# Optimization experiments

Measured on AMD Instinct MI355X. Metric: run time of the kernel, lower is better.

## Reference

```python
import jax, jax.numpy as jnp
import numpy as np

H_IMG = W_IMG = 1024
H_MAP = W_MAP = 64
SCALE = 16  # img // fmap, both axes
SCALES = [2, 2.5, 3, 3.5, 4, 5]
RATIOS = [0.5, 1.5, 2.0, 2.5, 3, 3.5, 4]
A = len(SCALES) * len(RATIOS)  # 42
POS_T, NEG_T = 0.5, 0.3


def _anchors_np():
    # generate_base_anchors + generate_anchor_boxes (down_h = down_w = SCALE)
    base = np.zeros((A, 4), np.float32)
    cy = cx = SCALE / 2.0
    i = 0
    for s in SCALES:
        for ar in RATIOS:
            h = SCALE * s * np.sqrt(ar)
            w = SCALE * s * np.sqrt(1.0 / ar)
            base[i] = [cy - h / 2.0, cx - w / 2.0, cy + h / 2.0, cx + w / 2.0]
            i += 1
    sy = np.arange(H_MAP) * SCALE
    sx = np.arange(W_MAP) * SCALE
    gx, gy = np.meshgrid(sx, sy)
    shifts = np.stack([gy.ravel(), gx.ravel(), gy.ravel(), gx.ravel()], axis=1)
    # order (H, W, A) -> matches conf.permute(0,2,3,1) flatten
    return (base[None, :, :] + shifts[:, None, :]).reshape(-1, 4).astype(np.float32)


def _conv(x, w, b):
    y = jax.lax.conv_general_dilated(x, w, (1, 1), 'SAME',
                                     dimension_numbers=('NCHW', 'OIHW', 'NCHW'))
    return y + b[None, :, None, None]


def setup_inputs() -> dict:
    key = jax.random.key(0)
    ks = jax.random.split(key, 10)
    B, N, C, Hm, Wm, HID = 8, 20, 256, 64, 64, 512
    feature_map = jax.random.normal(ks[0], (B, C, Hm, Wm), dtype=jnp.float32)
    # valid GT boxes in pixel xyxy-style (d0<d2, d1<d3), last 5 per image padded -1
    p0 = jax.random.uniform(ks[1], (B, N)) * 860.0
    p1 = jax.random.uniform(ks[2], (B, N)) * 860.0
    s0 = jax.random.uniform(ks[3], (B, N)) * 144.0 + 16.0
    s1 = jax.random.uniform(ks[4], (B, N)) * 144.0 + 16.0
    gt_bboxes = jnp.stack([p0, p1, p0 + s0, p1 + s1], axis=-1)
    gt_bboxes = gt_bboxes.at[:, 15:, :].set(-1.0)
    gt_classes = jax.random.randint(ks[5], (B, N), 0, 10)
    conv1_w = jax.random.normal(ks[6], (HID, C, 3, 3), dtype=jnp.float32) * 0.02
    conv1_b = jnp.zeros((HID,), jnp.float32)
    conf_w = jax.random.normal(ks[7], (A, HID, 1, 1), dtype=jnp.float32) * 0.02
    conf_b = jnp.zeros((A,), jnp.float32)
    reg_w = jax.random.normal(ks[8], (4 * A, HID, 1, 1), dtype=jnp.float32) * 0.02
    reg_b = jnp.zeros((4 * A,), jnp.float32)
    return {"feature_map": feature_map, "gt_bboxes": gt_bboxes, "gt_classes": gt_classes,
            "conv1_w": conv1_w, "conv1_b": conv1_b, "conf_w": conf_w, "conf_b": conf_b,
            "reg_w": reg_w, "reg_b": reg_b}


def reference(feature_map, gt_bboxes, gt_classes, conv1_w, conv1_b,
              conf_w, conf_b, reg_w, reg_b):
    anc = jnp.asarray(_anchors_np())           # [M,4]
    B = feature_map.shape[0]
    M = anc.shape[0]                           # H*W*A

    # project_bboxes p2a: divide by scale, keep -1 padding
    pad = gt_bboxes == -1.0
    g = jnp.where(pad, -1.0, gt_bboxes / float(SCALE))  # [B,N,4]
    valid = g[..., 0] >= 0                                # [B,N]
    g_safe = jnp.where(valid[..., None], g, jnp.array([0.0, 0.0, 1.0, 1.0]))

    # pairwise IoU [B,M,N] (vectorized get_iou_mat; invalid GT -> 0)
    tl = jnp.maximum(anc[None, :, None, :2], g_safe[:, None, :, :2])
    br = jnp.minimum(anc[None, :, None, 2:], g_safe[:, None, :, 2:])
    wh = jnp.clip(br - tl, 0.0)
    inter = wh[..., 0] * wh[..., 1]
    area_a = (anc[:, 2] - anc[:, 0]) * (anc[:, 3] - anc[:, 1])
    area_g = (g_safe[..., 2] - g_safe[..., 0]) * (g_safe[..., 3] - g_safe[..., 1])
    iou = inter / (area_a[None, :, None] + area_g[:, None, :] - inter)
    iou = jnp.where(valid[:, None, :], iou, 0.0)

    # positive assignment: per-GT argmax anchors + IoU > pos_thresh
    max_per_gt = iou.max(axis=1, keepdims=True)            # [B,1,N]
    pos_mask = ((iou == max_per_gt) & (max_per_gt > 0)) | (iou > POS_T)
    pos_any = pos_mask.any(axis=-1)                        # [B,M]
    a2g = jnp.argmax(iou, axis=2)                          # [B,M]
    max_per_anc = iou.max(axis=2)                          # [B,M]

    gt_for_anc = jnp.take_along_axis(g_safe, a2g[:, :, None], axis=1)  # [B,M,4]
    anc_b = jnp.broadcast_to(anc, (B, M, 4))
    gt_sel = jnp.where(pos_any[..., None], gt_for_anc, anc_b)  # safe for log

    # calc_gt_offsets (cxcywh encode), computed for all anchors, masked later
    a_c = (anc_b[..., :2] + anc_b[..., 2:]) * 0.5
    a_s = anc_b[..., 2:] - anc_b[..., :2]
    g_c = (gt_sel[..., :2] + gt_sel[..., 2:]) * 0.5
    g_s = gt_sel[..., 2:] - gt_sel[..., :2]
    off_gt = jnp.concatenate([(g_c - a_c) / a_s, jnp.log(g_s / a_s)], axis=-1)
    off_gt = off_gt.reshape(-1, 4)                          # [B*M,4]

    # ProposalModule head (dropout is a no-op in eval)
    x = jax.nn.relu(_conv(feature_map, conv1_w, conv1_b))
    conf = _conv(x, conf_w, conf_b)                         # [B,A,H,W]
    reg = _conv(x, reg_w, reg_b)                            # [B,4A,H,W]
    cflat = conf.transpose(0, 2, 3, 1).reshape(-1)          # [B*M]
    offp = reg.transpose(0, 2, 3, 1).reshape(-1, 4)         # [B*M,4]

    pf = pos_any.reshape(-1).astype(jnp.float32)
    P = pf.sum()

    # cls loss: BCE-with-logits, label 1 on positives, 0 on P sampled negatives
    cls_pos = (jax.nn.softplus(-cflat) * pf).sum() / P
    neg = max_per_anc.reshape(-1) < NEG_T
    scores = jax.random.uniform(jax.random.key(7), cflat.shape)
    scores = jnp.where(neg, scores, 2.0)
    ranks = jnp.argsort(jnp.argsort(scores))               # random sample = rank < P
    sel = (neg & (ranks < P)).astype(jnp.float32)
    cls_neg = (jax.nn.softplus(cflat) * sel).sum() / sel.sum()
    cls_loss = 0.5 * (cls_pos + cls_neg)

    d = offp - off_gt
    ad = jnp.abs(d)
    sl1 = jnp.where(ad < 1.0, 0.5 * ad * ad, ad - 0.5)
    reg_loss = (sl1 * pf[:, None]).sum() / (P * 4.0)

    return cls_loss + reg_loss
```

## Files before the change

### kernel.cpp

```cpp
#include <hip/hip_runtime.h>
#include <hip/hip_fp16.h>
#include <stdint.h>

constexpr int B_  = 8, HM = 64, WM = 64, A_ = 42, CIN = 256, HIDN = 512;
constexpr int M_  = HM * WM * A_;
constexpr int NA  = B_ * M_;
constexpr int HALF = NA / 2;
constexpr int KK  = CIN * 9;
constexpr float POS_T = 0.5f;

constexpr int WINY = 10, WINX = 10, WPIX = WINY * WINX;
constexpr int PERIMG = A_ * WPIX;
constexpr int WBLK = (PERIMG + 511) / 512;
constexpr int NMAXB = WBLK * B_;

constexpr int MAXPOS = 4096, MAXSEL = 4096, MAXCAND = 16384, MAXTIE = 256;
constexpr int MAXPIX = 1024;
constexpr uint32_t VCAND = 16384u;

constexpr int KSPL = 8, KCH = KK / KSPL;
constexpr int NSTRIP = MAXPIX / 64;
constexpr int NOCH = 4;
constexpr int NTILE = NSTRIP * NOCH * KSPL;
constexpr int TFBLK = HALF / 512;
constexpr int WCVTB = (HIDN * KK / 4) / 512;

constexpr size_t OFF_CTRL  = 0;
constexpr size_t OFF_BINS  = 256;
constexpr size_t OFF_MAXGT = 768;
constexpr size_t MS_END    = 1408;
constexpr size_t OFF_SLOT  = 2048;
constexpr size_t OFF_PLIST = 133120;
constexpr size_t OFF_POSL  = 137216;
constexpr size_t OFF_SELL  = 153600;
constexpr size_t OFF_CAND  = 169984;
constexpr size_t OFF_PART  = 301056;
constexpr size_t OFF_APATCH= 8689664;
constexpr size_t OFF_WF16  = 13408256;


__device__ __forceinline__ unsigned short f2bf(float f) {
  uint32_t x = __float_as_uint(f);
  uint32_t r = x + 0x7FFFu + ((x >> 16) & 1u);
  return (unsigned short)(r >> 16);
}
__device__ __forceinline__ float bf2f(unsigned short h) {
  return __uint_as_float(((uint32_t)h) << 16);
}
__device__ __forceinline__ uint32_t f2h2(float a, float b) {
  return (uint32_t)__half_as_ushort(__float2half_rn(a)) |
         ((uint32_t)__half_as_ushort(__float2half_rn(b)) << 16);
}

typedef _Float16 h8v __attribute__((ext_vector_type(8)));
typedef float f4v __attribute__((ext_vector_type(4)));

__device__ __forceinline__ float iou_pair(float ay0, float ax0, float ay1, float ax1,
                                          float areaA, float g0, float g1, float g2, float g3,
                                          float areaG) {
#pragma clang fp contract(off)
  float ty = fmaxf(ay0, g0), tx = fmaxf(ax0, g1);
  float by = fminf(ay1, g2), bx = fminf(ax1, g3);
  float hy = by - ty; hy = fmaxf(hy, 0.f);
  float hx = bx - tx; hx = fmaxf(hx, 0.f);
  float inter = hy * hx;
  return inter / (areaA + areaG - inter);
}

__device__ __forceinline__ void anchor_box(const float* basef, int a, int y, int x,
                                           float& ay0, float& ax0, float& ay1, float& ax1,
                                           float& areaA) {
#pragma clang fp contract(off)
  double sy = 16.0 * (double)y, sx = 16.0 * (double)x;
  ay0 = (float)((double)basef[a * 4 + 0] + sy);
  ax0 = (float)((double)basef[a * 4 + 1] + sx);
  ay1 = (float)((double)basef[a * 4 + 2] + sy);
  ax1 = (float)((double)basef[a * 4 + 3] + sx);
  areaA = (ay1 - ay0) * (ax1 - ax0);
}

__device__ __forceinline__ void fill_base(float* sbase, int t) {
  if (t < 42) {
    const double SC[6] = {2.0, 2.5, 3.0, 3.5, 4.0, 5.0};
    const double RA[7] = {0.5, 1.5, 2.0, 2.5, 3.0, 3.5, 4.0};
    int si = t / 7, ri = t - si * 7;
    double h = 16.0 * SC[si] * sqrt(RA[ri]);
    double w = 16.0 * SC[si] * sqrt(1.0 / RA[ri]);
    sbase[t * 4 + 0] = (float)(8.0 - h / 2.0);
    sbase[t * 4 + 1] = (float)(8.0 - w / 2.0);
    sbase[t * 4 + 2] = (float)(8.0 + h / 2.0);
    sbase[t * 4 + 3] = (float)(8.0 + w / 2.0);
  }
}

__device__ __forceinline__ void fill_gt(const float* gt, int b, float* sg, float* sarea,
                                        unsigned* sval, int t) {
  if (t < 20) {
#pragma clang fp contract(off)
    float g4[4];
    for (int d = 0; d < 4; d++) {
      float v = gt[(b * 20 + t) * 4 + d];
      g4[d] = (v == -1.0f) ? -1.0f : v * 0.0625f;
    }
    unsigned valid = (g4[0] >= 0.0f) ? 1u : 0u;
    if (!valid) { g4[0] = 0.f; g4[1] = 0.f; g4[2] = 1.f; g4[3] = 1.f; }
    sg[t * 4 + 0] = g4[0]; sg[t * 4 + 1] = g4[1]; sg[t * 4 + 2] = g4[2]; sg[t * 4 + 3] = g4[3];
    sarea[t] = (g4[2] - g4[0]) * (g4[3] - g4[1]);
    sval[t] = valid;
  }
}

__device__ __forceinline__ void claim_pixel(char* ws, int pixg) {
  int* slotmap = (int*)(ws + OFF_SLOT);
  if (atomicCAS((unsigned*)&slotmap[pixg], 0u, 0xFFFFFFFFu) == 0u) {
    unsigned s = atomicAdd((unsigned*)(ws + OFF_CTRL) + 2, 1u);
    if (s < MAXPIX) { ((int*)(ws + OFF_PLIST))[s] = pixg; slotmap[pixg] = (int)s + 1; }
    else slotmap[pixg] = -1;
  }
}

__device__ __forceinline__ float softplusf(float x) {
  return fmaxf(x, 0.f) + log1pf(expf(-fabsf(x)));
}
__device__ __forceinline__ float sl1(float d) {
  float ad = fabsf(d);
  return ad < 1.f ? 0.5f * ad * ad : ad - 0.5f;
}

__device__ __forceinline__ void tf_round(uint32_t& x0, uint32_t& x1, int r) {
  x0 += x1; x1 = (x1 << r) | (x1 >> (32 - r)); x1 ^= x0;
}
__device__ __forceinline__ void threefry(uint32_t c0, uint32_t c1, uint32_t& o0, uint32_t& o1) {
  const uint32_t k0 = 0u, k1 = 7u;
  const uint32_t k2 = k0 ^ k1 ^ 0x1BD11BDAu;
  uint32_t x0 = c0 + k0, x1 = c1 + k1;
  tf_round(x0, x1, 13); tf_round(x0, x1, 15); tf_round(x0, x1, 26); tf_round(x0, x1, 6);
  x0 += k1; x1 += k2 + 1u;
  tf_round(x0, x1, 17); tf_round(x0, x1, 29); tf_round(x0, x1, 16); tf_round(x0, x1, 24);
  x0 += k2; x1 += k0 + 2u;
  tf_round(x0, x1, 13); tf_round(x0, x1, 15); tf_round(x0, x1, 26); tf_round(x0, x1, 6);
  x0 += k0; x1 += k1 + 3u;
  tf_round(x0, x1, 17); tf_round(x0, x1, 29); tf_round(x0, x1, 16); tf_round(x0, x1, 24);
  x0 += k1; x1 += k2 + 4u;
  tf_round(x0, x1, 13); tf_round(x0, x1, 15); tf_round(x0, x1, 26); tf_round(x0, x1, 6);
  x0 += k2; x1 += k0 + 5u;
  o0 = x0; o1 = x1;
}

__device__ __forceinline__ void dev_threefry_emit(char* ws, int p) {
  uint32_t o0, o1; threefry((uint32_t)p, (uint32_t)(p + HALF), o0, o1);
  uint32_t v0 = o0 >> 9, v1 = o1 >> 9;
  unsigned* ctrl = (unsigned*)(ws + OFF_CTRL);
  unsigned* bins = (unsigned*)(ws + OFF_BINS);
  uint2* cand = (uint2*)(ws + OFF_CAND);
  if (v0 < VCAND) {
    unsigned s = atomicAdd(&ctrl[3], 1u);
    if (s < MAXCAND) cand[s] = make_uint2(v0, (unsigned)p);
    atomicAdd(&bins[v0 >> 7], 1u);
  }
  if (v1 < VCAND) {
    unsigned s = atomicAdd(&ctrl[3], 1u);
    if (s < MAXCAND) cand[s] = make_uint2(v1, (unsigned)(p + HALF));
    atomicAdd(&bins[v1 >> 7], 1u);
  }
}

__global__ void __launch_bounds__(512) kTF(const float* __restrict__ gt,
                                           const float* __restrict__ w1, char* ws) {
  __shared__ float sbase[168], sg[80], sarea[20];
  __shared__ unsigned sval[20];
  __shared__ int smax[20];
  int t = threadIdx.x;
  if (blockIdx.x < NMAXB) {
    int b = blockIdx.x / WBLK, blk = blockIdx.x - b * WBLK;
    fill_base(sbase, t);
    fill_gt(gt, b, sg, sarea, sval, t);
    if (t < 20) smax[t] = 0;
    __syncthreads();
    int idx = blk * 512 + t;
    bool ok = idx < PERIMG;
    float ay0 = 0.f, ax0 = 0.f, ay1 = 0.f, ax1 = 0.f, areaA = 1.f;
    if (ok) {
      int a = idx / WPIX, pp = idx - a * WPIX;
      int y = pp / WINX, x = pp - y * WINX;
      anchor_box(sbase, a, y, x, ay0, ax0, ay1, ax1, areaA);
    }
#pragma unroll
    for (int n = 0; n < 20; n++) {
      float io = 0.f;
      if (ok && sval[n]) io = iou_pair(ay0, ax0, ay1, ax1, areaA,
                                       sg[n * 4], sg[n * 4 + 1], sg[n * 4 + 2],
                                       sg[n * 4 + 3], sarea[n]);
#pragma unroll
      for (int off = 32; off >= 1; off >>= 1) io = fmaxf(io, __shfl_xor(io, off, 64));
      if ((t & 63) == 0 && io > 0.f) atomicMax(&smax[n], __float_as_int(io));
    }
    __syncthreads();
    if (t < 20 && smax[t] != 0)
      atomicMax((int*)(ws + OFF_MAXGT) + b * 20 + t, smax[t]);
  } else if (blockIdx.x < NMAXB + TFBLK) {
    int p = ((int)blockIdx.x - NMAXB) * 512 + t;
    if (p < 32768) ((int*)(ws + OFF_SLOT))[p] = 0;
    if (p < HALF) dev_threefry_emit(ws, p);
  } else {
    int q = ((int)blockIdx.x - (NMAXB + TFBLK)) * 512 + t;
    float4 v = ((const float4*)w1)[q];
    uint2 o;
    o.x = f2h2(v.x, v.y);
    o.y = f2h2(v.z, v.w);
    ((uint2*)(ws + OFF_WF16))[q] = o;
  }
}

__global__ void __launch_bounds__(512) kPos2(const float* __restrict__ gt, char* ws) {
  __shared__ float sbase[168], sg[80], sarea[20], smg[20];
  __shared__ unsigned sval[20];
  int b = blockIdx.y, t = threadIdx.x;
  unsigned* ctrl = (unsigned*)(ws + OFF_CTRL);
  fill_base(sbase, t);
  fill_gt(gt, b, sg, sarea, sval, t);
  if (t < 20) smg[t] = __int_as_float(((int*)(ws + OFF_MAXGT))[b * 20 + t]);
  __syncthreads();
  int idx = blockIdx.x * 512 + t;
  bool pos = false;
  unsigned packv = 0;
  int pixg = 0;
  if (idx < PERIMG) {
    int a = idx / WPIX, pp = idx - a * WPIX;
    int y = pp / WINX, x = pp - y * WINX;
    float ay0, ax0, ay1, ax1, areaA;
    anchor_box(sbase, a, y, x, ay0, ax0, ay1, ax1, areaA);
    float best = -1.f; int arg = 0;
#pragma unroll
    for (int n = 0; n < 20; n++) {
      float io = 0.f;
      if (sval[n]) io = iou_pair(ay0, ax0, ay1, ax1, areaA,
                                 sg[n * 4], sg[n * 4 + 1], sg[n * 4 + 2],
                                 sg[n * 4 + 3], sarea[n]);
      if (io > best) { best = io; arg = n; }
      float mg = smg[n];
      pos = pos || ((io == mg) && (mg > 0.f)) || (io > POS_T);
    }
    if (pos) {
      int pix = y * 64 + x;
      int i = b * M_ + pix * 42 + a;
      packv = (unsigned)i | ((unsigned)arg << 21);
      pixg = b * 4096 + pix;
    }
  }
  unsigned long long mask = __ballot(pos);
  if (mask) {
    int lane = t & 63;
    int leader = (int)__ffsll(mask) - 1;
    int cnt = __popcll(mask);
    unsigned base = 0;
    if (lane == leader) base = atomicAdd(&ctrl[0], (unsigned)cnt);
    base = (unsigned)__shfl((int)base, leader, 64);
    if (pos) {
      unsigned slot = base + (unsigned)__popcll(mask & ((1ull << lane) - 1ull));
      if (slot < MAXPOS) ((unsigned*)(ws + OFF_POSL))[slot] = packv;
      claim_pixel(ws, pixg);
    }
  }
}

__global__ void __launch_bounds__(1024) kSel(char* ws) {
  __shared__ unsigned selbins[128];
  __shared__ uint2 ties[MAXTIE];
  __shared__ unsigned tcnt, s_r, s_ucut;
  __shared__ int s_icut, s_cutbin;
  int t = threadIdx.x;
  unsigned* ctrl = (unsigned*)(ws + OFF_CTRL);
  const uint2* cand = (const uint2*)(ws + OFF_CAND);
  unsigned P = min(ctrl[0], (unsigned)MAXPOS);
  unsigned nc = min(ctrl[3], (unsigned)MAXCAND);
  if (t < 128) selbins[t] = ((const unsigned*)(ws + OFF_BINS))[t];
  if (t == 0) tcnt = 0;
  __syncthreads();
  if (t == 0) {
    unsigned cum = 0; int c = 0;
    for (; c < 128; c++) { if (cum + selbins[c] >= P) break; cum += selbins[c]; }
    if (c == 128) c = 127;
    s_cutbin = c; s_r = (P > cum) ? (P - cum) : 0u;
  }
  __syncthreads();
  int cutbin = s_cutbin;
  for (unsigned j = t; j < nc; j += 1024) {
    uint2 cj = cand[j];
    if ((int)(cj.x >> 7) == cutbin) {
      unsigned k = atomicAdd(&tcnt, 1u);
      if (k < MAXTIE) ties[k] = cj;
    }
  }
  __syncthreads();
  unsigned n = min(tcnt, (unsigned)MAXTIE);
  unsigned r = s_r; if (r > n) r = n;
  if (r == 0) {
    if (t == 0) { s_ucut = 0; s_icut = -1; }
  } else if (t < (int)n) {
    uint2 mine = ties[t];
    unsigned rank = 0;
    for (unsigned j = 0; j < n; j++) {
      uint2 o = ties[j];
      if (o.x < mine.x || (o.x == mine.x && (int)o.y < (int)mine.y)) rank++;
    }
    if (rank == r - 1) { s_ucut = mine.x; s_icut = (int)mine.y; }
  }
  __syncthreads();
  unsigned ucut = s_ucut; int icut = s_icut;
  unsigned total = (nc + 1023u) & ~1023u;
  for (unsigned j = t; j < total; j += 1024) {
    bool sel = false; uint2 cj = make_uint2(0u, 0u);
    if (j < nc) {
      cj = cand[j];
      sel = (cj.x < ucut) || (cj.x == ucut && (int)cj.y <= icut);
    }
    unsigned long long mask = __ballot(sel);
    if (mask) {
      int lane = t & 63;
      int leader = (int)__ffsll(mask) - 1;
      int cnt = __popcll(mask);
      unsigned base = 0;
      if (lane == leader) base = atomicAdd(&ctrl[1], (unsigned)cnt);
      base = (unsigned)__shfl((int)base, leader, 64);
      if (sel) {
        unsigned slot = base + (unsigned)__popcll(mask & ((1ull << lane) - 1ull));
        if (slot < MAXSEL) {
          ((int*)(ws + OFF_SELL))[slot] = (int)cj.y;
          int bb = (int)cj.y / M_; int m = (int)cj.y - bb * M_;
          claim_pixel(ws, bb * 4096 + m / 42);
        }
      }
    }
  }
}

__global__ void __launch_bounds__(256) kIm2col(const float* __restrict__ fm, char* ws) {
  unsigned* ctrl = (unsigned*)(ws + OFF_CTRL);
  int npix = min((int)ctrl[2], MAXPIX);
  int blk = blockIdx.x;
  if (blk >= npix) return;
  int chunk = blockIdx.y;
  int pixg = ((const int*)(ws + OFF_PLIST))[blk];
  int b = pixg >> 12, pix = pixg & 4095;
  int y = pix >> 6, x = pix & 63;
  uint32_t* Ap = (uint32_t*)(ws + OFF_APATCH) + (size_t)blk * (KK / 2);
  int u0 = chunk * 384;
  for (int u = u0 + threadIdx.x; u < u0 + 384; u += 256) {
    float v[2];
#pragma unroll
    for (int h = 0; h < 2; h++) {
      int k = 2 * u + h;
      int ic = k / 9, r = k - ic * 9;
      int dy = r / 3, dx = r - dy * 3;
      int yy = y + dy - 1, xx = x + dx - 1;
      float vv = 0.f;
      if (yy >= 0 && yy < 64 && xx >= 0 && xx < 64)
        vv = fm[(((size_t)b * CIN + ic) * 64 + yy) * 64 + xx];
      v[h] = vv;
    }
    Ap[u] = f2h2(v[0], v[1]);
  }
}

__global__ void __launch_bounds__(256) kGemm(char* ws) {
  unsigned* ctrl = (unsigned*)(ws + OFF_CTRL);
  int npix = min((int)ctrl[2], MAXPIX);
  int tile = blockIdx.x;
  int strip = tile & 15, r2 = tile >> 4;
  int och = r2 & 3, ks = r2 >> 2;
  int px0 = strip * 64;
  if (px0 >= npix) return;
  int oc0 = och * 128, kb = ks * KCH;
  const _Float16* Ap = (const _Float16*)(ws + OFF_APATCH);
  const _Float16* Wf = (const _Float16*)(ws + OFF_WF16);
  int t = threadIdx.x, lane = t & 63, wv = t >> 6;
  int kq = lane >> 4;
  const _Float16* Arow = Ap + (size_t)(px0 + wv * 16 + (lane & 15)) * KK + kb + kq * 8;
  const _Float16* Wrow = Wf + (size_t)(oc0 + (lane & 15)) * KK + kb + kq * 8;
  f4v acc[8] = {};
#pragma unroll 3
  for (int s = 0; s < 9; s++) {
    h8v a = *(const h8v*)(Arow + s * 32);
#pragma unroll
    for (int o = 0; o < 8; o++) {
      h8v bfr = *(const h8v*)(Wrow + (size_t)o * 16 * KK + s * 32);
      acc[o] = __builtin_amdgcn_mfma_f32_16x16x32_f16(a, bfr, acc[o], 0, 0, 0);
    }
  }
  unsigned short* part = (unsigned short*)(ws + OFF_PART) + (size_t)ks * MAXPIX * HIDN;
  int colbase = oc0 + (lane & 15);
  int pxb = px0 + wv * 16 + kq * 4;
#pragma unroll
  for (int o = 0; o < 8; o++) {
#pragma unroll
    for (int r = 0; r < 4; r++) {
      int px = pxb + r;
      if (px < npix)
        part[(size_t)px * HIDN + colbase + o * 16] = f2bf(acc[o][r]);
    }
  }
}

__global__ void __launch_bounds__(256) kHead(const float* __restrict__ gt,
                                             const float* __restrict__ b1,
                                             const float* __restrict__ cw,
                                             const float* __restrict__ cb,
                                             const float* __restrict__ rw,
                                             const float* __restrict__ rb,
                                             char* ws, float* out) {
  __shared__ float sbase[168], sg[640];
  __shared__ float sacc[3];
  int t = threadIdx.x;
  fill_base(sbase, t);
  if (t < 160) {
#pragma clang fp contract(off)
    float g4[4];
    for (int d = 0; d < 4; d++) {
      float v = gt[t * 4 + d];
      g4[d] = (v == -1.0f) ? -1.0f : v * 0.0625f;
    }
    if (!(g4[0] >= 0.0f)) { g4[0] = 0.f; g4[1] = 0.f; g4[2] = 1.f; g4[3] = 1.f; }
    sg[t * 4 + 0] = g4[0]; sg[t * 4 + 1] = g4[1];
    sg[t * 4 + 2] = g4[2]; sg[t * 4 + 3] = g4[3];
  }
  if (t < 3) sacc[t] = 0.f;
  __syncthreads();
  unsigned* ctrl = (unsigned*)(ws + OFF_CTRL);
  float* accum = (float*)(ctrl + 16);
  int np = min((int)ctrl[0], MAXPOS);
  int ns = min((int)ctrl[1], MAXSEL);
  int nent = np + ns;
  const unsigned* posl = (const unsigned*)(ws + OFF_POSL);
  const int* sell = (const int*)(ws + OFF_SELL);
  const int* slotmap = (const int*)(ws + OFF_SLOT);
  const unsigned short* part = (const unsigned short*)(ws + OFF_PART);
  constexpr size_t PS = (size_t)MAXPIX * HIDN;
  int lane = t & 63;
  int gwave = blockIdx.x * 4 + (t >> 6);
  int nwaves = gridDim.x * 4;
  for (int e = gwave; e < nent; e += nwaves) {
    bool isPos = e < np;
    int i, arg = 0;
    if (isPos) { unsigned pck = posl[e]; i = (int)(pck & 0x1FFFFFu); arg = (int)(pck >> 21); }
    else i = sell[e - np];
    int b = i / M_; int m = i - b * M_;
    int pix = m / 42; int a = m - pix * 42;
    int y = pix >> 6, x = pix & 63;
    int slot = slotmap[b * 4096 + pix] - 1;
    if (slot < 0 || slot >= MAXPIX) continue;
    float h[8];
    const unsigned short* pr = part + (size_t)slot * HIDN;
#pragma unroll
    for (int j = 0; j < 8; j++) {
      int c = lane + j * 64;
      float v = b1[c];
#pragma unroll
      for (int q = 0; q < KSPL; q++) v += bf2f(pr[c + q * PS]);
      h[j] = v > 0.f ? v : 0.f;
    }
    const float* cwr = cw + (size_t)a * HIDN;
    float cp = 0.f;
#pragma unroll
    for (int j = 0; j < 8; j++) cp += h[j] * cwr[lane + j * 64];
#pragma unroll
    for (int off = 32; off >= 1; off >>= 1) cp += __shfl_xor(cp, off, 64);
    float conf = cp + cb[a];
    if (isPos) {
      float rp[4];
#pragma unroll
      for (int d = 0; d < 4; d++) {
        const float* rwr = rw + (size_t)(a * 4 + d) * HIDN;
        float sd = 0.f;
#pragma unroll
        for (int j = 0; j < 8; j++) sd += h[j] * rwr[lane + j * 64];
#pragma unroll
        for (int off = 32; off >= 1; off >>= 1) sd += __shfl_xor(sd, off, 64);
        rp[d] = sd + rb[a * 4 + d];
      }
      if (lane == 0) {
#pragma clang fp contract(off)
        float ay0, ax0, ay1, ax1, areaA;
        anchor_box(sbase, a, y, x, ay0, ax0, ay1, ax1, areaA);
        const float* g = sg + (size_t)(b * 20 + arg) * 4;
        float acy = (ay0 + ay1) * 0.5f, acx = (ax0 + ax1) * 0.5f;
        float ah = ay1 - ay0, aw = ax1 - ax0;
        float gcy = (g[0] + g[2]) * 0.5f, gcx = (g[1] + g[3]) * 0.5f;
        float gh = g[2] - g[0], gw = g[3] - g[1];
        float t0 = (gcy - acy) / ah, t1 = (gcx - acx) / aw;
        float t2 = logf(gh / ah), t3 = logf(gw / aw);
        float sL = sl1(rp[0] - t0) + sl1(rp[1] - t1) + sl1(rp[2] - t2) + sl1(rp[3] - t3);
        atomicAdd(&sacc[2], sL);
        atomicAdd(&sacc[0], softplusf(-conf));
      }
    } else {
      if (lane == 0) atomicAdd(&sacc[1], softplusf(conf));
    }
  }
  __syncthreads();
  if (t == 0) {
    if (sacc[0] != 0.f) atomicAdd(&accum[0], sacc[0]);
    if (sacc[1] != 0.f) atomicAdd(&accum[1], sacc[1]);
    if (sacc[2] != 0.f) atomicAdd(&accum[2], sacc[2]);
    __threadfence();
    unsigned done = atomicAdd(&ctrl[10], 1u);
    if (done == gridDim.x - 1) {
      __threadfence();
      float P = (float)min((int)ctrl[0], MAXPOS);
      float S = (float)min((int)ctrl[1], MAXSEL);
      float cls = 0.5f * (accum[0] / P + accum[1] / S);
      out[0] = cls + accum[2] / (P * 4.0f);
    }
  }
}

extern "C" void kernel_launch(void* const* d_in, const int* in_sizes, int n_in,
                              void* d_out, int out_size, void* d_ws, size_t ws_size,
                              hipStream_t stream) {
  const float* fm = (const float*)d_in[0];
  const float* gt = (const float*)d_in[1];
  const float* w1 = (const float*)d_in[3];
  const float* b1 = (const float*)d_in[4];
  const float* cw = (const float*)d_in[5];
  const float* cb = (const float*)d_in[6];
  const float* rw = (const float*)d_in[7];
  const float* rb = (const float*)d_in[8];
  char* ws = (char*)d_ws;
  float* out = (float*)d_out;

  hipMemsetAsync(ws, 0, MS_END, stream);
  kTF<<<NMAXB + TFBLK + WCVTB, 512, 0, stream>>>(gt, w1, ws);
  kPos2<<<dim3(WBLK, B_), 512, 0, stream>>>(gt, ws);
  kSel<<<1, 1024, 0, stream>>>(ws);
  kIm2col<<<dim3(MAXPIX, 3), 256, 0, stream>>>(fm, ws);
  kGemm<<<NTILE, 256, 0, stream>>>(ws);
  kHead<<<128, 256, 0, stream>>>(gt, b1, cw, cb, rw, rb, ws, out);
}
```

Before: 182.1 us.

## Fuse positive-anchor and selection stages into first kernel via last-block completion counters

Merges kPos2 and kSel into kTF: the last block per image computes positive anchors once all per-GT max reductions are in, and the globally last block runs negative sampling. The slot map is now cleared by a larger memset. kGemm gains a last-split-block reduction that sums the K-split partials, adds bias, applies ReLU and writes fp16 hidden activations. kHead then reads these with vector loads instead of reducing eight partials per entry. Threefry candidate emission uses wave-aggregated atomics. This removes two launches and repeated reductions, at the cost of serial tail work in single blocks and extra fences.

```diff
diff --git a/kernel.cpp b/kernel.cpp
--- a/kernel.cpp
+++ b/kernel.cpp
@@ -24,12 +24,14 @@
 constexpr int NTILE = NSTRIP * NOCH * KSPL;
 constexpr int TFBLK = HALF / 512;
 constexpr int WCVTB = (HIDN * KK / 4) / 512;
+constexpr int NBLK_TF = NMAXB + TFBLK + WCVTB;
 
 constexpr size_t OFF_CTRL  = 0;
 constexpr size_t OFF_BINS  = 256;
 constexpr size_t OFF_MAXGT = 768;
-constexpr size_t MS_END    = 1408;
+constexpr size_t OFF_TDONE = 1408;
 constexpr size_t OFF_SLOT  = 2048;
+constexpr size_t MS_END    = 133120;
 constexpr size_t OFF_PLIST = 133120;
 constexpr size_t OFF_POSL  = 137216;
 constexpr size_t OFF_SELL  = 153600;
@@ -37,6 +39,7 @@
 constexpr size_t OFF_PART  = 301056;
 constexpr size_t OFF_APATCH= 8689664;
 constexpr size_t OFF_WF16  = 13408256;
+constexpr size_t OFF_HFIN  = 15767552;
 
 
 __device__ __forceinline__ unsigned short f2bf(float f) {
@@ -147,30 +150,46 @@
   o0 = x0; o1 = x1;
 }
 
-__device__ __forceinline__ void dev_threefry_emit(char* ws, int p) {
+__device__ __forceinline__ void dev_threefry_emit(char* ws, int p, int lane) {
   uint32_t o0, o1; threefry((uint32_t)p, (uint32_t)(p + HALF), o0, o1);
   uint32_t v0 = o0 >> 9, v1 = o1 >> 9;
   unsigned* ctrl = (unsigned*)(ws + OFF_CTRL);
   unsigned* bins = (unsigned*)(ws + OFF_BINS);
   uint2* cand = (uint2*)(ws + OFF_CAND);
-  if (v0 < VCAND) {
-    unsigned s = atomicAdd(&ctrl[3], 1u);
-    if (s < MAXCAND) cand[s] = make_uint2(v0, (unsigned)p);
-    atomicAdd(&bins[v0 >> 7], 1u);
-  }
-  if (v1 < VCAND) {
-    unsigned s = atomicAdd(&ctrl[3], 1u);
-    if (s < MAXCAND) cand[s] = make_uint2(v1, (unsigned)(p + HALF));
-    atomicAdd(&bins[v1 >> 7], 1u);
+  bool h0 = v0 < VCAND, h1 = v1 < VCAND;
+  unsigned long long m0 = __ballot(h0), m1 = __ballot(h1);
+  if (m0 | m1) {
+    int n0 = __popcll(m0);
+    int leader = (int)__ffsll(m0 | m1) - 1;
+    unsigned base = 0;
+    if (lane == leader) base = atomicAdd(&ctrl[3], (unsigned)(n0 + __popcll(m1)));
+    base = (unsigned)__shfl((int)base, leader, 64);
+    unsigned long long below = (1ull << lane) - 1ull;
+    if (h0) {
+      unsigned s = base + (unsigned)__popcll(m0 & below);
+      if (s < MAXCAND) cand[s] = make_uint2(v0, (unsigned)p);
+      atomicAdd(&bins[v0 >> 7], 1u);
+    }
+    if (h1) {
+      unsigned s = base + (unsigned)n0 + (unsigned)__popcll(m1 & below);
+      if (s < MAXCAND) cand[s] = make_uint2(v1, (unsigned)(p + HALF));
+      atomicAdd(&bins[v1 >> 7], 1u);
+    }
   }
 }
 
 __global__ void __launch_bounds__(512) kTF(const float* __restrict__ gt,
                                            const float* __restrict__ w1, char* ws) {
-  __shared__ float sbase[168], sg[80], sarea[20];
+  __shared__ float sbase[168], sg[80], sarea[20], smg[20];
   __shared__ unsigned sval[20];
   __shared__ int smax[20];
-  int t = threadIdx.x;
+  __shared__ int s_pos, s_sel;
+  __shared__ unsigned selbins[128];
+  __shared__ uint2 ties[MAXTIE];
+  __shared__ unsigned tcnt, s_r, s_ucut;
+  __shared__ int s_icut, s_cutbin;
+  int t = threadIdx.x, lane = t & 63;
+  unsigned* ctrl = (unsigned*)(ws + OFF_CTRL);
   if (blockIdx.x < NMAXB) {
     int b = blockIdx.x / WBLK, blk = blockIdx.x - b * WBLK;
     fill_base(sbase, t);
@@ -198,10 +217,55 @@
     __syncthreads();
     if (t < 20 && smax[t] != 0)
       atomicMax((int*)(ws + OFF_MAXGT) + b * 20 + t, smax[t]);
+    __threadfence();
+    if (t == 0) {
+      unsigned r = atomicAdd(&ctrl[24 + b], 1u);
+      s_pos = (r == (unsigned)WBLK - 1) ? 1 : 0;
+    }
+    __syncthreads();
+    if (s_pos) {
+      __threadfence();
+      if (t < 20) smg[t] = __int_as_float(((int*)(ws + OFF_MAXGT))[b * 20 + t]);
+      __syncthreads();
+      for (int i0 = t; i0 < PERIMG; i0 += 512) {
+        int a = i0 / WPIX, pp = i0 - a * WPIX;
+        int y = pp / WINX, x = pp - y * WINX;
+        float by0, bx0, by1, bx1, arA;
+        anchor_box(sbase, a, y, x, by0, bx0, by1, bx1, arA);
+        float best = -1.f; int arg = 0; bool pos = false;
+#pragma unroll
+        for (int n = 0; n < 20; n++) {
+          float io = 0.f;
+          if (sval[n]) io = iou_pair(by0, bx0, by1, bx1, arA,
+                                     sg[n * 4], sg[n * 4 + 1], sg[n * 4 + 2],
+                                     sg[n * 4 + 3], sarea[n]);
+          if (io > best) { best = io; arg = n; }
+          float mg = smg[n];
+          pos = pos || ((io == mg) && (mg > 0.f)) || (io > POS_T);
+        }
+        unsigned packv = 0; int pixg = 0;
+        if (pos) {
+          int pix = y * 64 + x;
+          packv = (unsigned)(b * M_ + pix * 42 + a) | ((unsigned)arg << 21);
+          pixg = b * 4096 + pix;
+        }
+        unsigned long long mask = __ballot(pos);
+        if (mask) {
+          int leader = (int)__ffsll(mask) - 1;
+          unsigned base = 0;
+          if (lane == leader) base = atomicAdd(&ctrl[0], (unsigned)__popcll(mask));
+          base = (unsigned)__shfl((int)base, leader, 64);
+          if (pos) {
+            unsigned slot = base + (unsigned)__popcll(mask & ((1ull << lane) - 1ull));
+            if (slot < MAXPOS) ((unsigned*)(ws + OFF_POSL))[slot] = packv;
+            claim_pixel(ws, pixg);
+          }
+        }
+      }
+    }
   } else if (blockIdx.x < NMAXB + TFBLK) {
     int p = ((int)blockIdx.x - NMAXB) * 512 + t;
-    if (p < 32768) ((int*)(ws + OFF_SLOT))[p] = 0;
-    if (p < HALF) dev_threefry_emit(ws, p);
+    if (p < HALF) dev_threefry_emit(ws, p, lane);
   } else {
     int q = ((int)blockIdx.x - (NMAXB + TFBLK)) * 512 + t;
     float4 v = ((const float4*)w1)[q];
@@ -210,67 +274,14 @@
     o.y = f2h2(v.z, v.w);
     ((uint2*)(ws + OFF_WF16))[q] = o;
   }
-}
-
-__global__ void __launch_bounds__(512) kPos2(const float* __restrict__ gt, char* ws) {
-  __shared__ float sbase[168], sg[80], sarea[20], smg[20];
-  __shared__ unsigned sval[20];
-  int b = blockIdx.y, t = threadIdx.x;
-  unsigned* ctrl = (unsigned*)(ws + OFF_CTRL);
-  fill_base(sbase, t);
-  fill_gt(gt, b, sg, sarea, sval, t);
-  if (t < 20) smg[t] = __int_as_float(((int*)(ws + OFF_MAXGT))[b * 20 + t]);
-  __syncthreads();
-  int idx = blockIdx.x * 512 + t;
-  bool pos = false;
-  unsigned packv = 0;
-  int pixg = 0;
-  if (idx < PERIMG) {
-    int a = idx / WPIX, pp = idx - a * WPIX;
-    int y = pp / WINX, x = pp - y * WINX;
-    float ay0, ax0, ay1, ax1, areaA;
-    anchor_box(sbase, a, y, x, ay0, ax0, ay1, ax1, areaA);
-    float best = -1.f; int arg = 0;
-#pragma unroll
-    for (int n = 0; n < 20; n++) {
-      float io = 0.f;
-      if (sval[n]) io = iou_pair(ay0, ax0, ay1, ax1, areaA,
-                                 sg[n * 4], sg[n * 4 + 1], sg[n * 4 + 2],
-                                 sg[n * 4 + 3], sarea[n]);
-      if (io > best) { best = io; arg = n; }
-      float mg = smg[n];
-      pos = pos || ((io == mg) && (mg > 0.f)) || (io > POS_T);
-    }
-    if (pos) {
-      int pix = y * 64 + x;
-      int i = b * M_ + pix * 42 + a;
-      packv = (unsigned)i | ((unsigned)arg << 21);
-      pixg = b * 4096 + pix;
-    }
-  }
-  unsigned long long mask = __ballot(pos);
-  if (mask) {
-    int lane = t & 63;
-    int leader = (int)__ffsll(mask) - 1;
-    int cnt = __popcll(mask);
-    unsigned base = 0;
-    if (lane == leader) base = atomicAdd(&ctrl[0], (unsigned)cnt);
-    base = (unsigned)__shfl((int)base, leader, 64);
-    if (pos) {
-      unsigned slot = base + (unsigned)__popcll(mask & ((1ull << lane) - 1ull));
-      if (slot < MAXPOS) ((unsigned*)(ws + OFF_POSL))[slot] = packv;
-      claim_pixel(ws, pixg);
-    }
-  }
-}
-
-__global__ void __launch_bounds__(1024) kSel(char* ws) {
-  __shared__ unsigned selbins[128];
-  __shared__ uint2 ties[MAXTIE];
-  __shared__ unsigned tcnt, s_r, s_ucut;
-  __shared__ int s_icut, s_cutbin;
-  int t = threadIdx.x;
-  unsigned* ctrl = (unsigned*)(ws + OFF_CTRL);
+  __threadfence();
+  if (t == 0) {
+    unsigned r = atomicAdd(&ctrl[11], 1u);
+    s_sel = (r == (unsigned)NBLK_TF - 1) ? 1 : 0;
+  }
+  __syncthreads();
+  if (!s_sel) return;
+  __threadfence();
   const uint2* cand = (const uint2*)(ws + OFF_CAND);
   unsigned P = min(ctrl[0], (unsigned)MAXPOS);
   unsigned nc = min(ctrl[3], (unsigned)MAXCAND);
@@ -285,7 +296,7 @@
   }
   __syncthreads();
   int cutbin = s_cutbin;
-  for (unsigned j = t; j < nc; j += 1024) {
+  for (unsigned j = t; j < nc; j += 512) {
     uint2 cj = cand[j];
     if ((int)(cj.x >> 7) == cutbin) {
       unsigned k = atomicAdd(&tcnt, 1u);
@@ -308,8 +319,8 @@
   }
   __syncthreads();
   unsigned ucut = s_ucut; int icut = s_icut;
-  unsigned total = (nc + 1023u) & ~1023u;
-  for (unsigned j = t; j < total; j += 1024) {
+  unsigned total = (nc + 511u) & ~511u;
+  for (unsigned j = t; j < total; j += 512) {
     bool sel = false; uint2 cj = make_uint2(0u, 0u);
     if (j < nc) {
       cj = cand[j];
@@ -317,11 +328,9 @@
     }
     unsigned long long mask = __ballot(sel);
     if (mask) {
-      int lane = t & 63;
       int leader = (int)__ffsll(mask) - 1;
-      int cnt = __popcll(mask);
       unsigned base = 0;
-      if (lane == leader) base = atomicAdd(&ctrl[1], (unsigned)cnt);
+      if (lane == leader) base = atomicAdd(&ctrl[1], (unsigned)__popcll(mask));
       base = (unsigned)__shfl((int)base, leader, 64);
       if (sel) {
         unsigned slot = base + (unsigned)__popcll(mask & ((1ull << lane) - 1ull));
@@ -363,12 +372,13 @@
   }
 }
 
-__global__ void __launch_bounds__(256) kGemm(char* ws) {
+__global__ void __launch_bounds__(256) kGemm(const float* __restrict__ b1, char* ws) {
+  __shared__ int s_red;
   unsigned* ctrl = (unsigned*)(ws + OFF_CTRL);
   int npix = min((int)ctrl[2], MAXPIX);
   int tile = blockIdx.x;
-  int strip = tile & 15, r2 = tile >> 4;
-  int och = r2 & 3, ks = r2 >> 2;
+  int strip = tile & 15, rr = tile >> 4;
+  int och = rr & 3, ks = rr >> 2;
   int px0 = strip * 64;
   if (px0 >= npix) return;
   int oc0 = och * 128, kb = ks * KCH;
@@ -388,7 +398,8 @@
       acc[o] = __builtin_amdgcn_mfma_f32_16x16x32_f16(a, bfr, acc[o], 0, 0, 0);
     }
   }
-  unsigned short* part = (unsigned short*)(ws + OFF_PART) + (size_t)ks * MAXPIX * HIDN;
+  constexpr size_t PS = (size_t)MAXPIX * HIDN;
+  unsigned short* part = (unsigned short*)(ws + OFF_PART) + (size_t)ks * PS;
   int colbase = oc0 + (lane & 15);
   int pxb = px0 + wv * 16 + kq * 4;
 #pragma unroll
@@ -399,6 +410,41 @@
       if (px < npix)
         part[(size_t)px * HIDN + colbase + o * 16] = f2bf(acc[o][r]);
     }
+  }
+  __threadfence();
+  if (t == 0) {
+    unsigned r = atomicAdd((unsigned*)(ws + OFF_TDONE) + (strip * 4 + och), 1u);
+    s_red = (r == (unsigned)KSPL - 1) ? 1 : 0;
+  }
+  __syncthreads();
+  if (!s_red) return;
+  __threadfence();
+  const unsigned short* p0 = (const unsigned short*)(ws + OFF_PART);
+  unsigned short* hf = (unsigned short*)(ws + OFF_HFIN);
+#pragma unroll
+  for (int i = 0; i < 4; i++) {
+    int c = t + 256 * i;
+    int px = c >> 4, ocg = c & 15;
+    size_t off = (size_t)(px0 + px) * HIDN + oc0 + ocg * 8;
+    float s8[8];
+#pragma unroll
+    for (int j = 0; j < 8; j++) s8[j] = b1[oc0 + ocg * 8 + j];
+#pragma unroll
+    for (int q = 0; q < KSPL; q++) {
+      uint4 v = *(const uint4*)(p0 + q * PS + off);
+      uint32_t a4[4] = {v.x, v.y, v.z, v.w};
+#pragma unroll
+      for (int w2 = 0; w2 < 4; w2++) {
+        s8[2 * w2]     += bf2f((unsigned short)(a4[w2] & 0xFFFFu));
+        s8[2 * w2 + 1] += bf2f((unsigned short)(a4[w2] >> 16));
+      }
+    }
+#pragma unroll
+    for (int j = 0; j < 8; j++) s8[j] = s8[j] > 0.f ? s8[j] : 0.f;
+    uint4 o;
+    o.x = f2h2(s8[0], s8[1]); o.y = f2h2(s8[2], s8[3]);
+    o.z = f2h2(s8[4], s8[5]); o.w = f2h2(s8[6], s8[7]);
+    *(uint4*)(hf + off) = o;
   }
 }
 
@@ -434,8 +480,7 @@
   const unsigned* posl = (const unsigned*)(ws + OFF_POSL);
   const int* sell = (const int*)(ws + OFF_SELL);
   const int* slotmap = (const int*)(ws + OFF_SLOT);
-  const unsigned short* part = (const unsigned short*)(ws + OFF_PART);
-  constexpr size_t PS = (size_t)MAXPIX * HIDN;
+  const unsigned short* hfin = (const unsigned short*)(ws + OFF_HFIN);
   int lane = t & 63;
   int gwave = blockIdx.x * 4 + (t >> 6);
   int nwaves = gridDim.x * 4;
@@ -450,19 +495,16 @@
     int slot = slotmap[b * 4096 + pix] - 1;
     if (slot < 0 || slot >= MAXPIX) continue;
     float h[8];
-    const unsigned short* pr = part + (size_t)slot * HIDN;
-#pragma unroll
-    for (int j = 0; j < 8; j++) {
-      int c = lane + j * 64;
-      float v = b1[c];
-#pragma unroll
-      for (int q = 0; q < KSPL; q++) v += bf2f(pr[c + q * PS]);
-      h[j] = v > 0.f ? v : 0.f;
-    }
-    const float* cwr = cw + (size_t)a * HIDN;
-    float cp = 0.f;
-#pragma unroll
-    for (int j = 0; j < 8; j++) cp += h[j] * cwr[lane + j * 64];
+    {
+      h8v hv = *(const h8v*)(hfin + (size_t)slot * HIDN + lane * 8);
+#pragma unroll
+      for (int j = 0; j < 8; j++) h[j] = (float)hv[j];
+    }
+    const float* cwr = cw + (size_t)a * HIDN + lane * 8;
+    float4 cA = *(const float4*)cwr;
+    float4 cB = *(const float4*)(cwr + 4);
+    float cp = h[0] * cA.x + h[1] * cA.y + h[2] * cA.z + h[3] * cA.w +
+               h[4] * cB.x + h[5] * cB.y + h[6] * cB.z + h[7] * cB.w;
 #pragma unroll
     for (int off = 32; off >= 1; off >>= 1) cp += __shfl_xor(cp, off, 64);
     float conf = cp + cb[a];
@@ -470,10 +512,11 @@
       float rp[4];
 #pragma unroll
       for (int d = 0; d < 4; d++) {
-        const float* rwr = rw + (size_t)(a * 4 + d) * HIDN;
-        float sd = 0.f;
-#pragma unroll
-        for (int j = 0; j < 8; j++) sd += h[j] * rwr[lane + j * 64];
+        const float* rwr = rw + (size_t)(a * 4 + d) * HIDN + lane * 8;
+        float4 rA = *(const float4*)rwr;
+        float4 rB = *(const float4*)(rwr + 4);
+        float sd = h[0] * rA.x + h[1] * rA.y + h[2] * rA.z + h[3] * rA.w +
+                   h[4] * rB.x + h[5] * rB.y + h[6] * rB.z + h[7] * rB.w;
 #pragma unroll
         for (int off = 32; off >= 1; off >>= 1) sd += __shfl_xor(sd, off, 64);
         rp[d] = sd + rb[a * 4 + d];
@@ -529,10 +572,8 @@
   float* out = (float*)d_out;
 
   hipMemsetAsync(ws, 0, MS_END, stream);
-  kTF<<<NMAXB + TFBLK + WCVTB, 512, 0, stream>>>(gt, w1, ws);
-  kPos2<<<dim3(WBLK, B_), 512, 0, stream>>>(gt, ws);
-  kSel<<<1, 1024, 0, stream>>>(ws);
+  kTF<<<NBLK_TF, 512, 0, stream>>>(gt, w1, ws);
   kIm2col<<<dim3(MAXPIX, 3), 256, 0, stream>>>(fm, ws);
-  kGemm<<<NTILE, 256, 0, stream>>>(ws);
-  kHead<<<128, 256, 0, stream>>>(gt, b1, cw, cb, rw, rb, ws, out);
-}
+  kGemm<<<NTILE, 256, 0, stream>>>(b1, ws);
+  kHead<<<256, 256, 0, stream>>>(gt, b1, cw, cb, rw, rb, ws, out);
+}
```

Result: slower. 476.5 us (+161.7%).

## Pre-reduce split-K partials per pixel and batch threefry candidate atomics per wave

Applied to the files above, without the earlier changes.

Adds a kReduce kernel that sums the eight bf16 split-K partials once per claimed pixel, applies bias and ReLU, and stores fp16 hidden vectors. kHead then reads eight contiguous halves per lane with vector loads instead of re-reducing the partials for every anchor entry. The threefry candidate emission now does one wave-aggregated atomic instead of one per candidate, and the slot-map zeroing moves into the memset, which grows accordingly. The head grid is doubled. The cost is an extra kernel launch and an extra round trip through global memory for the hidden vectors.

```diff
diff --git a/kernel.cpp b/kernel.cpp
--- a/kernel.cpp
+++ b/kernel.cpp
@@ -24,12 +24,13 @@
 constexpr int NTILE = NSTRIP * NOCH * KSPL;
 constexpr int TFBLK = HALF / 512;
 constexpr int WCVTB = (HIDN * KK / 4) / 512;
+constexpr int NBLK_TF = NMAXB + TFBLK + WCVTB;
 
 constexpr size_t OFF_CTRL  = 0;
 constexpr size_t OFF_BINS  = 256;
 constexpr size_t OFF_MAXGT = 768;
-constexpr size_t MS_END    = 1408;
 constexpr size_t OFF_SLOT  = 2048;
+constexpr size_t MS_END    = 133120;
 constexpr size_t OFF_PLIST = 133120;
 constexpr size_t OFF_POSL  = 137216;
 constexpr size_t OFF_SELL  = 153600;
@@ -37,6 +38,7 @@
 constexpr size_t OFF_PART  = 301056;
 constexpr size_t OFF_APATCH= 8689664;
 constexpr size_t OFF_WF16  = 13408256;
+constexpr size_t OFF_HFIN  = 15767552;
 
 
 __device__ __forceinline__ unsigned short f2bf(float f) {
@@ -147,21 +149,31 @@
   o0 = x0; o1 = x1;
 }
 
-__device__ __forceinline__ void dev_threefry_emit(char* ws, int p) {
+__device__ __forceinline__ void dev_threefry_emit(char* ws, int p, int lane) {
   uint32_t o0, o1; threefry((uint32_t)p, (uint32_t)(p + HALF), o0, o1);
   uint32_t v0 = o0 >> 9, v1 = o1 >> 9;
   unsigned* ctrl = (unsigned*)(ws + OFF_CTRL);
   unsigned* bins = (unsigned*)(ws + OFF_BINS);
   uint2* cand = (uint2*)(ws + OFF_CAND);
-  if (v0 < VCAND) {
-    unsigned s = atomicAdd(&ctrl[3], 1u);
-    if (s < MAXCAND) cand[s] = make_uint2(v0, (unsigned)p);
-    atomicAdd(&bins[v0 >> 7], 1u);
-  }
-  if (v1 < VCAND) {
-    unsigned s = atomicAdd(&ctrl[3], 1u);
-    if (s < MAXCAND) cand[s] = make_uint2(v1, (unsigned)(p + HALF));
-    atomicAdd(&bins[v1 >> 7], 1u);
+  bool h0 = v0 < VCAND, h1 = v1 < VCAND;
+  unsigned long long m0 = __ballot(h0), m1 = __ballot(h1);
+  if (m0 | m1) {
+    int n0 = __popcll(m0);
+    int leader = (int)__ffsll(m0 | m1) - 1;
+    unsigned base = 0;
+    if (lane == leader) base = atomicAdd(&ctrl[3], (unsigned)(n0 + __popcll(m1)));
+    base = (unsigned)__shfl((int)base, leader, 64);
+    unsigned long long below = (1ull << lane) - 1ull;
+    if (h0) {
+      unsigned s = base + (unsigned)__popcll(m0 & below);
+      if (s < MAXCAND) cand[s] = make_uint2(v0, (unsigned)p);
+      atomicAdd(&bins[v0 >> 7], 1u);
+    }
+    if (h1) {
+      unsigned s = base + (unsigned)n0 + (unsigned)__popcll(m1 & below);
+      if (s < MAXCAND) cand[s] = make_uint2(v1, (unsigned)(p + HALF));
+      atomicAdd(&bins[v1 >> 7], 1u);
+    }
   }
 }
 
@@ -170,7 +182,7 @@
   __shared__ float sbase[168], sg[80], sarea[20];
   __shared__ unsigned sval[20];
   __shared__ int smax[20];
-  int t = threadIdx.x;
+  int t = threadIdx.x, lane = t & 63;
   if (blockIdx.x < NMAXB) {
     int b = blockIdx.x / WBLK, blk = blockIdx.x - b * WBLK;
     fill_base(sbase, t);
@@ -200,8 +212,7 @@
       atomicMax((int*)(ws + OFF_MAXGT) + b * 20 + t, smax[t]);
   } else if (blockIdx.x < NMAXB + TFBLK) {
     int p = ((int)blockIdx.x - NMAXB) * 512 + t;
-    if (p < 32768) ((int*)(ws + OFF_SLOT))[p] = 0;
-    if (p < HALF) dev_threefry_emit(ws, p);
+    if (p < HALF) dev_threefry_emit(ws, p, lane);
   } else {
     int q = ((int)blockIdx.x - (NMAXB + TFBLK)) * 512 + t;
     float4 v = ((const float4*)w1)[q];
@@ -252,9 +263,8 @@
   if (mask) {
     int lane = t & 63;
     int leader = (int)__ffsll(mask) - 1;
-    int cnt = __popcll(mask);
     unsigned base = 0;
-    if (lane == leader) base = atomicAdd(&ctrl[0], (unsigned)cnt);
+    if (lane == leader) base = atomicAdd(&ctrl[0], (unsigned)__popcll(mask));
     base = (unsigned)__shfl((int)base, leader, 64);
     if (pos) {
       unsigned slot = base + (unsigned)__popcll(mask & ((1ull << lane) - 1ull));
@@ -319,9 +329,8 @@
     if (mask) {
       int lane = t & 63;
       int leader = (int)__ffsll(mask) - 1;
-      int cnt = __popcll(mask);
       unsigned base = 0;
-      if (lane == leader) base = atomicAdd(&ctrl[1], (unsigned)cnt);
+      if (lane == leader) base = atomicAdd(&ctrl[1], (unsigned)__popcll(mask));
       base = (unsigned)__shfl((int)base, leader, 64);
       if (sel) {
         unsigned slot = base + (unsigned)__popcll(mask & ((1ull << lane) - 1ull));
@@ -402,8 +411,28 @@
   }
 }
 
+__global__ void __launch_bounds__(256) kReduce(const float* __restrict__ b1, char* ws) {
+  unsigned* ctrl = (unsigned*)(ws + OFF_CTRL);
+  int npix = min((int)ctrl[2], MAXPIX);
+  int px = blockIdx.x;
+  if (px >= npix) return;
+  int t = threadIdx.x;
+  constexpr size_t PS = (size_t)MAXPIX * HIDN;
+  const unsigned short* p0 = (const unsigned short*)(ws + OFF_PART);
+  unsigned short* hf = (unsigned short*)(ws + OFF_HFIN);
+  size_t off = (size_t)px * HIDN + t * 2;
+  float s0 = b1[t * 2], s1 = b1[t * 2 + 1];
+#pragma unroll
+  for (int q = 0; q < KSPL; q++) {
+    uint32_t v = *(const uint32_t*)(p0 + q * PS + off);
+    s0 += bf2f((unsigned short)(v & 0xFFFFu));
+    s1 += bf2f((unsigned short)(v >> 16));
+  }
+  s0 = fmaxf(s0, 0.f); s1 = fmaxf(s1, 0.f);
+  *(uint32_t*)(hf + off) = f2h2(s0, s1);
+}
+
 __global__ void __launch_bounds__(256) kHead(const float* __restrict__ gt,
-                                             const float* __restrict__ b1,
                                              const float* __restrict__ cw,
                                              const float* __restrict__ cb,
                                              const float* __restrict__ rw,
@@ -434,8 +463,7 @@
   const unsigned* posl = (const unsigned*)(ws + OFF_POSL);
   const int* sell = (const int*)(ws + OFF_SELL);
   const int* slotmap = (const int*)(ws + OFF_SLOT);
-  const unsigned short* part = (const unsigned short*)(ws + OFF_PART);
-  constexpr size_t PS = (size_t)MAXPIX * HIDN;
+  const unsigned short* hfin = (const unsigned short*)(ws + OFF_HFIN);
   int lane = t & 63;
   int gwave = blockIdx.x * 4 + (t >> 6);
   int nwaves = gridDim.x * 4;
@@ -450,19 +478,16 @@
     int slot = slotmap[b * 4096 + pix] - 1;
     if (slot < 0 || slot >= MAXPIX) continue;
     float h[8];
-    const unsigned short* pr = part + (size_t)slot * HIDN;
-#pragma unroll
-    for (int j = 0; j < 8; j++) {
-      int c = lane + j * 64;
-      float v = b1[c];
-#pragma unroll
-      for (int q = 0; q < KSPL; q++) v += bf2f(pr[c + q * PS]);
-      h[j] = v > 0.f ? v : 0.f;
-    }
-    const float* cwr = cw + (size_t)a * HIDN;
-    float cp = 0.f;
-#pragma unroll
-    for (int j = 0; j < 8; j++) cp += h[j] * cwr[lane + j * 64];
+    {
+      h8v hv = *(const h8v*)(hfin + (size_t)slot * HIDN + lane * 8);
+#pragma unroll
+      for (int j = 0; j < 8; j++) h[j] = (float)hv[j];
+    }
+    const float* cwr = cw + (size_t)a * HIDN + lane * 8;
+    float4 cA = *(const float4*)cwr;
+    float4 cB = *(const float4*)(cwr + 4);
+    float cp = h[0] * cA.x + h[1] * cA.y + h[2] * cA.z + h[3] * cA.w +
+               h[4] * cB.x + h[5] * cB.y + h[6] * cB.z + h[7] * cB.w;
 #pragma unroll
     for (int off = 32; off >= 1; off >>= 1) cp += __shfl_xor(cp, off, 64);
     float conf = cp + cb[a];
@@ -470,10 +495,11 @@
       float rp[4];
 #pragma unroll
       for (int d = 0; d < 4; d++) {
-        const float* rwr = rw + (size_t)(a * 4 + d) * HIDN;
-        float sd = 0.f;
-#pragma unroll
-        for (int j = 0; j < 8; j++) sd += h[j] * rwr[lane + j * 64];
+        const float* rwr = rw + (size_t)(a * 4 + d) * HIDN + lane * 8;
+        float4 rA = *(const float4*)rwr;
+        float4 rB = *(const float4*)(rwr + 4);
+        float sd = h[0] * rA.x + h[1] * rA.y + h[2] * rA.z + h[3] * rA.w +
+                   h[4] * rB.x + h[5] * rB.y + h[6] * rB.z + h[7] * rB.w;
 #pragma unroll
         for (int off = 32; off >= 1; off >>= 1) sd += __shfl_xor(sd, off, 64);
         rp[d] = sd + rb[a * 4 + d];
@@ -529,10 +555,11 @@
   float* out = (float*)d_out;
 
   hipMemsetAsync(ws, 0, MS_END, stream);
-  kTF<<<NMAXB + TFBLK + WCVTB, 512, 0, stream>>>(gt, w1, ws);
+  kTF<<<NBLK_TF, 512, 0, stream>>>(gt, w1, ws);
   kPos2<<<dim3(WBLK, B_), 512, 0, stream>>>(gt, ws);
   kSel<<<1, 1024, 0, stream>>>(ws);
   kIm2col<<<dim3(MAXPIX, 3), 256, 0, stream>>>(fm, ws);
   kGemm<<<NTILE, 256, 0, stream>>>(ws);
-  kHead<<<128, 256, 0, stream>>>(gt, b1, cw, cb, rw, rb, ws, out);
-}
+  kReduce<<<MAXPIX, 256, 0, stream>>>(b1, ws);
+  kHead<<<256, 256, 0, stream>>>(gt, cw, cb, rw, rb, ws, out);
+}
```

Result: faster. 177.8 us (-2.3%).
